# Kernel optimization log

Hardware: AMD Instinct MI355X
Metric: run time of the kernel (lower is better)

## Reference

```python
import jax, jax.numpy as jnp
import numpy as np

B = 512       # batch_size
IN = 256      # input_size
H = 512       # hidden_size
OUT = 64      # output_size
N_PAIRS = B - 1   # number of H0 persistence deaths (connected components merges)
TOL = 1e-6    # rtol for torch.isclose
ATOL = 1e-8   # torch default atol
EPS = 0.0     # homology_eps
TARGET_P = 1.0
HOM_P = 1.0
COMP_P = 0.01

_IU = np.triu_indices(B, 1)  # condensed pdist indexing, static


def _mlp(batch, W1, b1, W2, b2, W3, b3, Wout, bout):
    # FeedForward: input->hidden, (n_layers-1) hidden->hidden, hidden->output, ReLU
    h = jax.nn.relu(batch @ W1 + b1)
    h = jax.nn.relu(h @ W2 + b2)
    h = jax.nn.relu(h @ W3 + b3)
    return h @ Wout + bout


def _pdist(y):
    # condensed euclidean pairwise distances, same ordering as torch F.pdist
    d = y[_IU[0]] - y[_IU[1]]                 # [P, OUT]
    return jnp.sqrt(jnp.sum(d * d, axis=-1))  # [P]


def setup_inputs() -> dict:
    key = jax.random.key(0)
    ks = jax.random.split(key, 8)
    batch = jax.random.normal(ks[0], (B, IN), jnp.float32)
    target = jax.random.normal(ks[1], (B, OUT), jnp.float32)
    W1 = jax.random.normal(ks[2], (IN, H), jnp.float32) / np.sqrt(IN)
    W2 = jax.random.normal(ks[3], (H, H), jnp.float32) / np.sqrt(H)
    W3 = jax.random.normal(ks[4], (H, H), jnp.float32) / np.sqrt(H)
    Wout = jax.random.normal(ks[5], (H, OUT), jnp.float32) / np.sqrt(H)
    b1 = jnp.zeros((H,), jnp.float32)
    b2 = jnp.zeros((H,), jnp.float32)
    b3 = jnp.zeros((H,), jnp.float32)
    bout = jnp.zeros((OUT,), jnp.float32)
    # persistence deaths = actual critical pdist values (from the external
    # Vietoris-Rips routine in the original); sample N_PAIRS distinct entries.
    y0 = _mlp(batch, W1, b1, W2, b2, W3, b3, Wout, bout)
    pd0 = np.asarray(_pdist(y0))
    idx = np.random.default_rng(0).choice(pd0.shape[0], N_PAIRS, replace=False)
    persistence_deaths = jnp.asarray(pd0[idx], jnp.float32)
    return {"batch": batch, "target": target,
            "W1": W1, "b1": b1, "W2": W2, "b2": b2, "W3": W3, "b3": b3,
            "Wout": Wout, "bout": bout,
            "persistence_deaths": persistence_deaths}


def reference(batch, target, W1, b1, W2, b2, W3, b3, Wout, bout, persistence_deaths):
    y = _mlp(batch, W1, b1, W2, b2, W3, b3, Wout, bout)   # [B, OUT]
    y_hom = y  # normalize_for_homology = False
    pd = _pdist(y_hom)                                     # [P]
    # vectorized indicator_death over all pairs (replaces per-pair Python loop)
    mask = jnp.any(jnp.isclose(pd[:, None], persistence_deaths[None, :],
                               rtol=TOL, atol=ATOL), axis=1)      # [P] bool
    # homology_dim=0: birth_pdist = 0; norm=1 of selected (death - 0 + eps)
    homology_loss = jnp.sum(jnp.abs(jnp.where(mask, pd + EPS, 0.0)))
    target_loss = jnp.mean((target - y) ** 2)
    compactness_loss = jnp.sum(jnp.abs(y - jnp.mean(y, axis=0, keepdims=True)))
    loss = TARGET_P * target_loss + HOM_P * homology_loss + COMP_P * compactness_loss
    return loss
```

## Files before the change

### kernel.cpp

```cpp
#include <hip/hip_runtime.h>

#define B_    512
#define IN_   256
#define H_    512
#define OUT_  64
#define NDEATH (B_ - 1)
#define NSORT  512
#define RTOL_ 1e-6
#define ATOL_ 1e-8
#define NBLK  256
#define KT    32

typedef __attribute__((ext_vector_type(4))) double d4_t;

__device__ __forceinline__ void ast(double* p, double v) {
    __hip_atomic_store(p, v, __ATOMIC_RELAXED, __HIP_MEMORY_SCOPE_AGENT);
}

__device__ __forceinline__ void gbar(unsigned* cnt, unsigned nb) {
    __syncthreads();
    if (threadIdx.x == 0) {
        __hip_atomic_fetch_add(cnt, 1u, __ATOMIC_RELAXED,
                               __HIP_MEMORY_SCOPE_AGENT);
        while (__hip_atomic_load(cnt, __ATOMIC_RELAXED,
                                 __HIP_MEMORY_SCOPE_AGENT) < nb)
            __builtin_amdgcn_s_sleep(2);
    }
    __syncthreads();
}

__device__ void sort_windows(const float* __restrict__ deaths,
                             double* sd, double* slo, double* shi, int t) {
    int i1 = t + 256;
    sd[t]  = (t  < NDEATH) ? (double)deaths[t]  : 1e300;
    sd[i1] = (i1 < NDEATH) ? (double)deaths[i1] : 1e300;
    __syncthreads();
    for (int k = 2; k <= NSORT; k <<= 1) {
        for (int j = k >> 1; j > 0; j >>= 1) {
            int l = ((t & ~(j - 1)) << 1) | (t & (j - 1));
            int p = l + j;
            bool up = ((l & k) == 0);
            double a = sd[l], b = sd[p];
            if ((a > b) == up) { sd[l] = b; sd[p] = a; }
            __syncthreads();
        }
    }
    for (int i = t; i < NSORT; i += 256) {
        double d = sd[i];
        double w = ATOL_ + RTOL_ * fabs(d);
        slo[i] = d - w;
        shi[i] = d + w;
    }
    __syncthreads();
}

template <typename TIN, bool RELU>
__device__ void gemm_dev(const TIN* __restrict__ A, const float* __restrict__ W,
                         const float* __restrict__ bias, double* __restrict__ C,
                         int N, int K, int tile, int t,
                         double (&As)[2][KT][33], double (&Ws)[2][KT][33]) {
    const int lane = t & 63;
    const int wave = t >> 6;
    const int wm   = wave & 1, wn = wave >> 1;
    const int nbx  = N >> 5;
    const int row0 = (tile / nbx) << 5;
    const int col0 = (tile % nbx) << 5;

    const int akk = t & 31;
    const int amm = t >> 5;
    const int wnn = t & 31;
    const int wkk = t >> 5;
    const int nkt = K >> 5;

    TIN   ar[2][4];
    float wr[2][4];

    auto load_to = [&](int rs, int kt) {
        const int k0 = kt << 5;
        #pragma unroll
        for (int p = 0; p < 4; ++p) {
            ar[rs][p] = A[(size_t)(row0 + amm + 8 * p) * K + k0 + akk];
            wr[rs][p] = W[(size_t)(k0 + wkk + 8 * p) * N + col0 + wnn];
        }
    };
    auto stage = [&](int rs, int buf) {
        #pragma unroll
        for (int p = 0; p < 4; ++p) {
            As[buf][akk][amm + 8 * p] = (double)ar[rs][p];
            Ws[buf][wkk + 8 * p][wnn] = (double)wr[rs][p];
        }
    };

    load_to(0, 0);
    if (nkt > 1) load_to(1, 1);
    stage(0, 0);
    __syncthreads();

    d4_t c4 = {0.0, 0.0, 0.0, 0.0};
    const int mrow = wm * 16 + (lane & 15);
    const int ncol = wn * 16 + (lane & 15);
    const int kq   = lane >> 4;

    for (int kt = 0; kt < nkt; ++kt) {
        const int cur = kt & 1;
        if (kt + 2 < nkt) load_to(cur, kt + 2);
        #pragma unroll
        for (int ks = 0; ks < KT / 4; ++ks) {
            double av = As[cur][ks * 4 + kq][mrow];
            double bv = Ws[cur][ks * 4 + kq][ncol];
            c4 = __builtin_amdgcn_mfma_f64_16x16x4f64(av, bv, c4, 0, 0, 0);
        }
        __syncthreads();
        if (kt + 1 < nkt) stage(cur ^ 1, cur ^ 1);
        __syncthreads();
    }

    #pragma unroll
    for (int r = 0; r < 4; ++r) {
        int row = row0 + wm * 16 + (lane >> 4) * 4 + r;
        int col = col0 + wn * 16 + (lane & 15);
        double v = c4[r] + (double)bias[col];
        if (RELU) v = v > 0.0 ? v : 0.0;
        ast(&C[(size_t)row * N + col], v);
    }
}

__device__ void mc_dev(const float* __restrict__ target,
                       const double* __restrict__ y,
                       double* __restrict__ t_part, double* __restrict__ c_part,
                       int c, int t) {
    const int wave = t >> 6, lane = t & 63;
    double v0 = y[(size_t)t * OUT_ + c];
    double v1 = y[(size_t)(t + 256) * OUT_ + c];
    double s = v0 + v1;
    for (int off = 32; off; off >>= 1) s += __shfl_down(s, off);
    __shared__ double swm[4];
    __shared__ double smean;
    if (lane == 0) swm[wave] = s;
    __syncthreads();
    if (t == 0) smean = (swm[0] + swm[1] + swm[2] + swm[3]) / (double)B_;
    __syncthreads();
    double m = smean;
    double d0 = (double)target[(size_t)t * OUT_ + c] - v0;
    double d1 = (double)target[(size_t)(t + 256) * OUT_ + c] - v1;
    double t_s = d0 * d0 + d1 * d1;
    double c_s = fabs(v0 - m) + fabs(v1 - m);
    for (int off = 32; off; off >>= 1) {
        t_s += __shfl_down(t_s, off);
        c_s += __shfl_down(c_s, off);
    }
    __shared__ double st[4], sc[4];
    if (lane == 0) { st[wave] = t_s; sc[wave] = c_s; }
    __syncthreads();
    if (t == 0) {
        ast(&t_part[c], st[0] + st[1] + st[2] + st[3]);
        ast(&c_part[c], sc[0] + sc[1] + sc[2] + sc[3]);
    }
}

__device__ __forceinline__ double pair_val(const double* __restrict__ yrow_s,
                                           const double* __restrict__ yj,
                                           const double* __restrict__ slo,
                                           const double* __restrict__ shi) {
    double s = 0.0;
    #pragma unroll
    for (int d = 0; d < OUT_; d += 2) {
        double2 v = *(const double2*)(yj + d);
        double d0 = yrow_s[d]     - v.x;
        double d1 = yrow_s[d + 1] - v.y;
        s = fma(d0, d0, s);
        s = fma(d1, d1, s);
    }
    double pd = sqrt(s);
    int pos = 0;
    #pragma unroll
    for (int step = NSORT / 2; step; step >>= 1) {
        if (slo[pos + step - 1] <= pd) pos += step;
    }
    bool m = (pos > 0) && (shi[pos - 1] >= pd);
    return m ? pd : 0.0;
}

__device__ void pdist_dev(const double* __restrict__ y,
                          double* __restrict__ hom_part, int bid, int t,
                          double* yA, double* yB,
                          const double* slo, const double* shi) {
    const int iA = bid;
    const int iB = 510 - bid;
    if (t < OUT_)            yA[t]        = y[(size_t)iA * OUT_ + t];
    else if (t < 2 * OUT_)   yB[t - OUT_] = y[(size_t)iB * OUT_ + (t - OUT_)];
    __syncthreads();

    double local = 0.0;
    for (int j = iA + 1 + t; j < B_; j += 256)
        local += pair_val(yA, y + (size_t)j * OUT_, slo, shi);
    if (iB != iA)
        for (int j = iB + 1 + t; j < B_; j += 256)
            local += pair_val(yB, y + (size_t)j * OUT_, slo, shi);

    for (int off = 32; off; off >>= 1) local += __shfl_down(local, off);
    __shared__ double sw[4];
    int wave = t >> 6, lane = t & 63;
    if (lane == 0) sw[wave] = local;
    __syncthreads();
    if (t == 0) ast(&hom_part[bid], sw[0] + sw[1] + sw[2] + sw[3]);
}

__global__ __launch_bounds__(256) void fused_k(
    const float* __restrict__ batch, const float* __restrict__ target,
    const float* __restrict__ W1, const float* __restrict__ b1,
    const float* __restrict__ W2, const float* __restrict__ b2,
    const float* __restrict__ W3, const float* __restrict__ b3,
    const float* __restrict__ Wout, const float* __restrict__ bout,
    const float* __restrict__ deaths, float* __restrict__ out,
    double* __restrict__ hA, double* __restrict__ hB,
    double* __restrict__ hC, double* __restrict__ yv,
    double* __restrict__ hom_part, double* __restrict__ t_part,
    double* __restrict__ c_part, unsigned* __restrict__ cnt) {
    const int bid = blockIdx.x;
    const int t   = threadIdx.x;
    const int g   = bid >> 4;
    const int c   = bid & 15;
    unsigned* gc  = cnt + g * 32;

    __shared__ double As[2][KT][33];
    __shared__ double Ws[2][KT][33];
    __shared__ double slo[NSORT], shi[NSORT];
    __shared__ double yA[OUT_], yB[OUT_];
    __shared__ int    lastf;
    double* sd = &As[0][0][0];

    gemm_dev<float,  true>(batch, W1, b1, hA, H_, IN_, bid, t, As, Ws);
    gbar(&gc[0], 16);
    gemm_dev<double, true>(hA, W2, b2, hB, H_, H_, bid, t, As, Ws);
    gbar(&gc[1], 16);
    gemm_dev<double, true>(hB, W3, b3, hC, H_, H_, bid, t, As, Ws);
    gbar(&gc[2], 16);

    if (c < 2) gemm_dev<double, false>(hC, Wout, bout, yv, OUT_, H_, g * 2 + c, t, As, Ws);
    else       sort_windows(deaths, sd, slo, shi, t);

    gbar(&cnt[512], NBLK);
    if (c < 2) sort_windows(deaths, sd, slo, shi, t);

    pdist_dev(yv, hom_part, bid, t, yA, yB, slo, shi);
    if (bid < OUT_) mc_dev(target, yv, t_part, c_part, bid, t);

    __syncthreads();
    if (t == 0) {
        unsigned prev = __hip_atomic_fetch_add(&cnt[544], 1u, __ATOMIC_RELAXED,
                                               __HIP_MEMORY_SCOPE_AGENT);
        lastf = (prev == NBLK - 1);
    }
    __syncthreads();
    if (lastf) {
        double h  = __hip_atomic_load(&hom_part[t], __ATOMIC_RELAXED,
                                      __HIP_MEMORY_SCOPE_AGENT);
        double tp = 0.0, cp = 0.0;
        if (t < OUT_) {
            tp = __hip_atomic_load(&t_part[t], __ATOMIC_RELAXED,
                                   __HIP_MEMORY_SCOPE_AGENT);
            cp = __hip_atomic_load(&c_part[t], __ATOMIC_RELAXED,
                                   __HIP_MEMORY_SCOPE_AGENT);
        }
        for (int off = 32; off; off >>= 1) {
            h  += __shfl_down(h,  off);
            tp += __shfl_down(tp, off);
            cp += __shfl_down(cp, off);
        }
        __shared__ double sh[4], stp[4], scp[4];
        int wave = t >> 6, lane = t & 63;
        if (lane == 0) { sh[wave] = h; stp[wave] = tp; scp[wave] = cp; }
        __syncthreads();
        if (t == 0) {
            double hs = sh[0]  + sh[1]  + sh[2]  + sh[3];
            double ts = stp[0] + stp[1] + stp[2] + stp[3];
            double cs = scp[0] + scp[1] + scp[2] + scp[3];
            out[0] = (float)(ts / (double)(B_ * OUT_) + hs + 0.01 * cs);
        }
    }
}

extern "C" void kernel_launch(void* const* d_in, const int* in_sizes, int n_in,
                              void* d_out, int out_size, void* d_ws, size_t ws_size,
                              hipStream_t stream) {
    const float* batch  = (const float*)d_in[0];
    const float* target = (const float*)d_in[1];
    const float* W1     = (const float*)d_in[2];
    const float* b1     = (const float*)d_in[3];
    const float* W2     = (const float*)d_in[4];
    const float* b2     = (const float*)d_in[5];
    const float* W3     = (const float*)d_in[6];
    const float* b3     = (const float*)d_in[7];
    const float* Wout   = (const float*)d_in[8];
    const float* bout   = (const float*)d_in[9];
    const float* deaths = (const float*)d_in[10];
    float* out = (float*)d_out;

    double* hA       = (double*)d_ws;
    double* hB       = hA + (size_t)B_ * H_;
    double* hC       = hB + (size_t)B_ * H_;
    double* yv       = hC + (size_t)B_ * H_;
    double* hom_part = yv + (size_t)B_ * OUT_;
    double* t_part   = hom_part + NBLK;
    double* c_part   = t_part + OUT_;
    unsigned* cnt    = (unsigned*)(c_part + OUT_);

    hipMemsetAsync(cnt, 0, 576 * sizeof(unsigned), stream);

    fused_k<<<dim3(NBLK), dim3(256), 0, stream>>>(
        batch, target, W1, b1, W2, b2, W3, b3, Wout, bout, deaths, out,
        hA, hB, hC, yv, hom_part, t_part, c_part, cnt);
}
```

Baseline: 133.7 us.

## Double block size and split K across two wave groups in fused GEMMs

```diff
diff --git a/kernel.cpp b/kernel.cpp
--- a/kernel.cpp
+++ b/kernel.cpp
@@ -9,6 +9,7 @@
 #define RTOL_ 1e-6
 #define ATOL_ 1e-8
 #define NBLK  256
+#define NTHR  512
 #define KT    32
 
 typedef __attribute__((ext_vector_type(4))) double d4_t;
@@ -31,25 +32,25 @@
 
 __device__ void sort_windows(const float* __restrict__ deaths,
                              double* sd, double* slo, double* shi, int t) {
-    int i1 = t + 256;
-    sd[t]  = (t  < NDEATH) ? (double)deaths[t]  : 1e300;
-    sd[i1] = (i1 < NDEATH) ? (double)deaths[i1] : 1e300;
+    if (t < NSORT) sd[t] = (t < NDEATH) ? (double)deaths[t] : 1e300;
     __syncthreads();
     for (int k = 2; k <= NSORT; k <<= 1) {
         for (int j = k >> 1; j > 0; j >>= 1) {
-            int l = ((t & ~(j - 1)) << 1) | (t & (j - 1));
-            int p = l + j;
-            bool up = ((l & k) == 0);
-            double a = sd[l], b = sd[p];
-            if ((a > b) == up) { sd[l] = b; sd[p] = a; }
+            if (t < 256) {
+                int l = ((t & ~(j - 1)) << 1) | (t & (j - 1));
+                int p = l + j;
+                bool up = ((l & k) == 0);
+                double a = sd[l], b = sd[p];
+                if ((a > b) == up) { sd[l] = b; sd[p] = a; }
+            }
             __syncthreads();
         }
     }
-    for (int i = t; i < NSORT; i += 256) {
-        double d = sd[i];
+    if (t < NSORT) {
+        double d = sd[t];
         double w = ATOL_ + RTOL_ * fabs(d);
-        slo[i] = d - w;
-        shi[i] = d + w;
+        slo[t] = d - w;
+        shi[t] = d + w;
     }
     __syncthreads();
 }
@@ -58,25 +59,28 @@
 __device__ void gemm_dev(const TIN* __restrict__ A, const float* __restrict__ W,
                          const float* __restrict__ bias, double* __restrict__ C,
                          int N, int K, int tile, int t,
-                         double (&As)[2][KT][33], double (&Ws)[2][KT][33]) {
-    const int lane = t & 63;
-    const int wave = t >> 6;
-    const int wm   = wave & 1, wn = wave >> 1;
-    const int nbx  = N >> 5;
-    const int row0 = (tile / nbx) << 5;
-    const int col0 = (tile % nbx) << 5;
-
-    const int akk = t & 31;
-    const int amm = t >> 5;
-    const int wnn = t & 31;
-    const int wkk = t >> 5;
-    const int nkt = K >> 5;
+                         double (&As)[2][2][KT][33], double (&Ws)[2][2][KT][33]) {
+    const int lane  = t & 63;
+    const int wave4 = (t >> 6) & 3;
+    const int w2    = t >> 8;
+    const int tg    = t & 255;
+    const int wm    = wave4 & 1, wn = wave4 >> 1;
+    const int nbx   = N >> 5;
+    const int row0  = (tile / nbx) << 5;
+    const int col0  = (tile % nbx) << 5;
+
+    const int akk   = tg & 31;
+    const int amm   = tg >> 5;
+    const int wnn   = tg & 31;
+    const int wkk   = tg >> 5;
+    const int kbase = w2 * (K >> 1);
+    const int nkt   = K >> 6;
 
     TIN   ar[2][4];
     float wr[2][4];
 
     auto load_to = [&](int rs, int kt) {
-        const int k0 = kt << 5;
+        const int k0 = kbase + (kt << 5);
         #pragma unroll
         for (int p = 0; p < 4; ++p) {
             ar[rs][p] = A[(size_t)(row0 + amm + 8 * p) * K + k0 + akk];
@@ -86,8 +90,8 @@
     auto stage = [&](int rs, int buf) {
         #pragma unroll
         for (int p = 0; p < 4; ++p) {
-            As[buf][akk][amm + 8 * p] = (double)ar[rs][p];
-            Ws[buf][wkk + 8 * p][wnn] = (double)wr[rs][p];
+            As[w2][buf][akk][amm + 8 * p] = (double)ar[rs][p];
+            Ws[w2][buf][wkk + 8 * p][wnn] = (double)wr[rs][p];
         }
     };
 
@@ -106,22 +110,31 @@
         if (kt + 2 < nkt) load_to(cur, kt + 2);
         #pragma unroll
         for (int ks = 0; ks < KT / 4; ++ks) {
-            double av = As[cur][ks * 4 + kq][mrow];
-            double bv = Ws[cur][ks * 4 + kq][ncol];
+            double av = As[w2][cur][ks * 4 + kq][mrow];
+            double bv = Ws[w2][cur][ks * 4 + kq][ncol];
             c4 = __builtin_amdgcn_mfma_f64_16x16x4f64(av, bv, c4, 0, 0, 0);
         }
-        __syncthreads();
         if (kt + 1 < nkt) stage(cur ^ 1, cur ^ 1);
         __syncthreads();
     }
 
-    #pragma unroll
-    for (int r = 0; r < 4; ++r) {
-        int row = row0 + wm * 16 + (lane >> 4) * 4 + r;
-        int col = col0 + wn * 16 + (lane & 15);
-        double v = c4[r] + (double)bias[col];
-        if (RELU) v = v > 0.0 ? v : 0.0;
-        ast(&C[(size_t)row * N + col], v);
+    double (*cEx)[16][17] = (double (*)[16][17])(&As[0][0][0][0]);
+    const int r4 = (lane >> 4) * 4;
+    if (w2 == 1) {
+        #pragma unroll
+        for (int r = 0; r < 4; ++r)
+            cEx[wave4][r4 + r][lane & 15] = c4[r];
+    }
+    __syncthreads();
+    if (w2 == 0) {
+        #pragma unroll
+        for (int r = 0; r < 4; ++r) {
+            int row = row0 + wm * 16 + r4 + r;
+            int col = col0 + wn * 16 + (lane & 15);
+            double v = c4[r] + cEx[wave4][r4 + r][lane & 15] + (double)bias[col];
+            if (RELU) v = v > 0.0 ? v : 0.0;
+            ast(&C[(size_t)row * N + col], v);
+        }
     }
 }
 
@@ -130,31 +143,37 @@
                        double* __restrict__ t_part, double* __restrict__ c_part,
                        int c, int t) {
     const int wave = t >> 6, lane = t & 63;
-    double v0 = y[(size_t)t * OUT_ + c];
-    double v1 = y[(size_t)(t + 256) * OUT_ + c];
-    double s = v0 + v1;
+    double v = y[(size_t)t * OUT_ + c];
+    double s = v;
     for (int off = 32; off; off >>= 1) s += __shfl_down(s, off);
-    __shared__ double swm[4];
+    __shared__ double swm[8];
     __shared__ double smean;
     if (lane == 0) swm[wave] = s;
     __syncthreads();
-    if (t == 0) smean = (swm[0] + swm[1] + swm[2] + swm[3]) / (double)B_;
+    if (t == 0) {
+        double m = 0.0;
+        #pragma unroll
+        for (int w = 0; w < 8; ++w) m += swm[w];
+        smean = m / (double)B_;
+    }
     __syncthreads();
     double m = smean;
-    double d0 = (double)target[(size_t)t * OUT_ + c] - v0;
-    double d1 = (double)target[(size_t)(t + 256) * OUT_ + c] - v1;
-    double t_s = d0 * d0 + d1 * d1;
-    double c_s = fabs(v0 - m) + fabs(v1 - m);
+    double d = (double)target[(size_t)t * OUT_ + c] - v;
+    double t_s = d * d;
+    double c_s = fabs(v - m);
     for (int off = 32; off; off >>= 1) {
         t_s += __shfl_down(t_s, off);
         c_s += __shfl_down(c_s, off);
     }
-    __shared__ double st[4], sc[4];
+    __shared__ double st[8], sc[8];
     if (lane == 0) { st[wave] = t_s; sc[wave] = c_s; }
     __syncthreads();
     if (t == 0) {
-        ast(&t_part[c], st[0] + st[1] + st[2] + st[3]);
-        ast(&c_part[c], sc[0] + sc[1] + sc[2] + sc[3]);
+        double ts = 0.0, cs = 0.0;
+        #pragma unroll
+        for (int w = 0; w < 8; ++w) { ts += st[w]; cs += sc[w]; }
+        ast(&t_part[c], ts);
+        ast(&c_part[c], cs);
     }
 }
 
@@ -192,21 +211,26 @@
     __syncthreads();
 
     double local = 0.0;
-    for (int j = iA + 1 + t; j < B_; j += 256)
+    for (int j = iA + 1 + t; j < B_; j += NTHR)
         local += pair_val(yA, y + (size_t)j * OUT_, slo, shi);
     if (iB != iA)
-        for (int j = iB + 1 + t; j < B_; j += 256)
+        for (int j = iB + 1 + t; j < B_; j += NTHR)
             local += pair_val(yB, y + (size_t)j * OUT_, slo, shi);
 
     for (int off = 32; off; off >>= 1) local += __shfl_down(local, off);
-    __shared__ double sw[4];
+    __shared__ double sw[8];
     int wave = t >> 6, lane = t & 63;
     if (lane == 0) sw[wave] = local;
     __syncthreads();
-    if (t == 0) ast(&hom_part[bid], sw[0] + sw[1] + sw[2] + sw[3]);
-}
-
-__global__ __launch_bounds__(256) void fused_k(
+    if (t == 0) {
+        double s = 0.0;
+        #pragma unroll
+        for (int w = 0; w < 8; ++w) s += sw[w];
+        ast(&hom_part[bid], s);
+    }
+}
+
+__global__ __launch_bounds__(NTHR) void fused_k(
     const float* __restrict__ batch, const float* __restrict__ target,
     const float* __restrict__ W1, const float* __restrict__ b1,
     const float* __restrict__ W2, const float* __restrict__ b2,
@@ -223,12 +247,12 @@
     const int c   = bid & 15;
     unsigned* gc  = cnt + g * 32;
 
-    __shared__ double As[2][KT][33];
-    __shared__ double Ws[2][KT][33];
+    __shared__ double As[2][2][KT][33];
+    __shared__ double Ws[2][2][KT][33];
     __shared__ double slo[NSORT], shi[NSORT];
     __shared__ double yA[OUT_], yB[OUT_];
     __shared__ int    lastf;
-    double* sd = &As[0][0][0];
+    double* sd = &As[0][0][0][0];
 
     gemm_dev<float,  true>(batch, W1, b1, hA, H_, IN_, bid, t, As, Ws);
     gbar(&gc[0], 16);
@@ -254,9 +278,10 @@
     }
     __syncthreads();
     if (lastf) {
-        double h  = __hip_atomic_load(&hom_part[t], __ATOMIC_RELAXED,
-                                      __HIP_MEMORY_SCOPE_AGENT);
-        double tp = 0.0, cp = 0.0;
+        double h = 0.0, tp = 0.0, cp = 0.0;
+        if (t < NBLK)
+            h = __hip_atomic_load(&hom_part[t], __ATOMIC_RELAXED,
+                                  __HIP_MEMORY_SCOPE_AGENT);
         if (t < OUT_) {
             tp = __hip_atomic_load(&t_part[t], __ATOMIC_RELAXED,
                                    __HIP_MEMORY_SCOPE_AGENT);
@@ -268,14 +293,16 @@
             tp += __shfl_down(tp, off);
             cp += __shfl_down(cp, off);
         }
-        __shared__ double sh[4], stp[4], scp[4];
+        __shared__ double sh[8], stp[8], scp[8];
         int wave = t >> 6, lane = t & 63;
         if (lane == 0) { sh[wave] = h; stp[wave] = tp; scp[wave] = cp; }
         __syncthreads();
         if (t == 0) {
-            double hs = sh[0]  + sh[1]  + sh[2]  + sh[3];
-            double ts = stp[0] + stp[1] + stp[2] + stp[3];
-            double cs = scp[0] + scp[1] + scp[2] + scp[3];
+            double hs = 0.0, ts = 0.0, cs = 0.0;
+            #pragma unroll
+            for (int w = 0; w < 8; ++w) {
+                hs += sh[w]; ts += stp[w]; cs += scp[w];
+            }
             out[0] = (float)(ts / (double)(B_ * OUT_) + hs + 0.01 * cs);
         }
     }
@@ -308,7 +335,7 @@
 
     hipMemsetAsync(cnt, 0, 576 * sizeof(unsigned), stream);
 
-    fused_k<<<dim3(NBLK), dim3(256), 0, stream>>>(
+    fused_k<<<dim3(NBLK), dim3(NTHR), 0, stream>>>(
         batch, target, W1, b1, W2, b2, W3, b3, Wout, bout, deaths, out,
         hA, hB, hC, yv, hom_part, t_part, c_part, cnt);
 }
```

Result: no change. 134.1 us (+0.3%).
